# Kernel tuning notes

Measured on AMD Instinct MI355X. Metric: run time of the kernel, lower is better.

The kernel has to match this reference:

```python
import jax, jax.numpy as jnp
import numpy as np

N, D_IN, D_OUT = 4096, 1024, 1024

def setup_inputs() -> dict:
    key = jax.random.key(0)
    ks = jax.random.split(key, 7)
    s = 1.0 / np.sqrt(D_IN)
    return {
        "x": jax.random.normal(ks[0], (N, D_IN), dtype=jnp.float32),
        "W1": jax.random.normal(ks[1], (D_OUT, D_IN), dtype=jnp.float32) * s,
        "b1": jax.random.normal(ks[2], (D_OUT,), dtype=jnp.float32) * 0.01,
        "W2": jax.random.normal(ks[3], (D_OUT, D_IN), dtype=jnp.float32) * s,
        "b2": jax.random.normal(ks[4], (D_OUT,), dtype=jnp.float32) * 0.01,
        "W3": jax.random.normal(ks[5], (D_OUT, D_IN), dtype=jnp.float32) * s,
        "b3": jax.random.normal(ks[6], (D_OUT,), dtype=jnp.float32) * 0.01,
        "output_dim": D_OUT,
    }

def reference(x, W1, b1, W2, b2, W3, b3, output_dim):
    # q, k, v: [N, D_OUT]  (torch Linear: x @ W.T + b)
    q = x @ W1.T + b1
    k = x @ W2.T + b2
    v = x @ W3.T + b3
    # NOTE: original computes K @ Q^T (not Q @ K^T) — keep faithful.
    scale = 1.0 / jnp.sqrt(jnp.asarray(output_dim, dtype=x.dtype))
    attn = jax.nn.softmax(jnp.einsum("nd,md->nm", k, q) * scale, axis=-1)  # [N, N]
    # value.unsqueeze(0) * attn.unsqueeze(-1) summed over axis 1 == attn @ v
    return attn @ v  # [N, D_OUT]
```

## Files before the change

### kernel.cpp

```cpp
#include <hip/hip_runtime.h>


typedef short bf16x8 __attribute__((ext_vector_type(8)));
typedef float f32x4  __attribute__((ext_vector_type(4)));

__device__ __forceinline__ short f2bf(float f) {
    unsigned u = __builtin_bit_cast(unsigned, f);
    u += 0x7FFFu + ((u >> 16) & 1u);
    return (short)(u >> 16);
}
__device__ __forceinline__ float bf2f(short s) {
    return __builtin_bit_cast(float, (unsigned)((unsigned short)s) << 16);
}

__device__ __forceinline__ void gld_lds16(const short* g, short* l) {
    __builtin_amdgcn_global_load_lds(
        (const __attribute__((address_space(1))) void*)g,
        (__attribute__((address_space(3))) void*)l, 16, 0, 0);
}

#define WAITV(n) asm volatile("s_waitcnt vmcnt(" #n ")" ::: "memory")
#define BAR() __builtin_amdgcn_s_barrier()

template<int CMODE>
__global__ __launch_bounds__(512)
void gemm256(const short* __restrict__ A, int lda,
             const short* __restrict__ B, int ldb,
             const float* __restrict__ bias,
             short* __restrict__ Cout, int ldc, float scale,
             int K, size_t zstride)
{
    __shared__ __align__(16) short As[2][2][128 * 64];
    __shared__ __align__(16) short Bs[2][2][128 * 64];

    const int tid  = threadIdx.x;
    const int lane = tid & 63;
    const int wave = tid >> 6;
    const int wr   = wave >> 2;
    const int wc   = wave & 3;
    const int quad = lane >> 4;
    const int l16  = lane & 15;
    const size_t bm0 = (size_t)blockIdx.y * 256;
    const size_t bn0 = (size_t)blockIdx.x * 256;
    const int koff = blockIdx.z * K;

    f32x4 acc[8][4] = {};

    const int srow  = lane >> 3;
    const int sgran = (lane & 7) ^ srow;
    const short* Ag0 = A + (bm0 + wave * 16 + srow) * (size_t)lda + koff + sgran * 8;
    const short* Ag1 = Ag0 + (size_t)128 * lda;
    const short* Bg0 = B + (bn0 + wave * 16 + srow) * (size_t)ldb + koff + sgran * 8;
    const short* Bg1 = Bg0 + (size_t)128 * ldb;

    const int s0  = ((quad ^ (l16 & 7)) << 3);
    const int s1  = (((4 + quad) ^ (l16 & 7)) << 3);
    const int rdA0 = (wr * 64 + l16) * 64;
    const int rdB0 = (wc * 32 + l16) * 64;

    const int NT = K >> 6;

    auto stage = [&](short* half, const short* g, int ld, int kt) {
#pragma unroll
        for (int i = 0; i < 2; ++i)
            gld_lds16(g + (size_t)(i * 8) * ld + kt,
                      half + (wave * 16 + i * 8) * 64);
    };

    bf16x8 af[4][2], bfr0[2][2], bfr1[2][2];

    auto ldAf = [&](const short* Ah) {
#pragma unroll
        for (int m4 = 0; m4 < 4; ++m4) {
            af[m4][0] = *(const bf16x8*)(Ah + rdA0 + m4 * 1024 + s0);
            af[m4][1] = *(const bf16x8*)(Ah + rdA0 + m4 * 1024 + s1);
        }
    };
    auto ldBf = [&](bf16x8 (&bx)[2][2], const short* Bh) {
#pragma unroll
        for (int n2 = 0; n2 < 2; ++n2) {
            bx[n2][0] = *(const bf16x8*)(Bh + rdB0 + n2 * 1024 + s0);
            bx[n2][1] = *(const bf16x8*)(Bh + rdB0 + n2 * 1024 + s1);
        }
    };
    auto mm = [&](int mq, int nq, bf16x8 (&bx)[2][2]) {
        __builtin_amdgcn_s_setprio(1);
#pragma unroll
        for (int ks = 0; ks < 2; ++ks)
#pragma unroll
            for (int m4 = 0; m4 < 4; ++m4)
#pragma unroll
                for (int n2 = 0; n2 < 2; ++n2)
                    acc[mq * 4 + m4][nq * 2 + n2] =
                        __builtin_amdgcn_mfma_f32_16x16x32_bf16(
                            af[m4][ks], bx[n2][ks],
                            acc[mq * 4 + m4][nq * 2 + n2], 0, 0, 0);
        __builtin_amdgcn_s_setprio(0);
    };

    stage(&As[0][0][0], Ag0, lda, 0);
    stage(&As[0][1][0], Ag1, lda, 0);
    stage(&Bs[0][0][0], Bg0, ldb, 0);
    stage(&Bs[0][1][0], Bg1, ldb, 0);
    stage(&As[1][0][0], Ag0, lda, 64);
    stage(&Bs[1][1][0], Bg1, ldb, 64);
    WAITV(4);
    BAR();
    __builtin_amdgcn_sched_barrier(0);

    for (int it = 0; it < NT / 2; ++it) {
        const int k1 = it * 128 + 64;
        const int k2 = it * 128 + 128;
        const int k3 = it * 128 + 192;
        const bool m2 = k2 < K, m3 = k3 < K;

        ldAf(&As[0][0][0]);
        ldBf(bfr0, &Bs[0][0][0]);
        stage(&As[1][1][0], Ag1, lda, k1);
        BAR();
        mm(0, 0, bfr0);
        ldBf(bfr1, &Bs[0][1][0]);
        stage(&Bs[1][0][0], Bg0, ldb, k1);
        BAR();
        mm(0, 1, bfr1);
        ldAf(&As[0][1][0]);
        if (m2) stage(&As[0][0][0], Ag0, lda, k2);
        BAR();
        mm(1, 1, bfr1);
        if (m2) stage(&Bs[0][1][0], Bg1, ldb, k2);
        mm(1, 0, bfr0);
        if (m2) { WAITV(4); } else { WAITV(0); }
        BAR();

        ldAf(&As[1][0][0]);
        ldBf(bfr0, &Bs[1][0][0]);
        if (m2) stage(&As[0][1][0], Ag1, lda, k2);
        BAR();
        mm(0, 0, bfr0);
        ldBf(bfr1, &Bs[1][1][0]);
        if (m2) stage(&Bs[0][0][0], Bg0, ldb, k2);
        BAR();
        mm(0, 1, bfr1);
        ldAf(&As[1][1][0]);
        if (m3) stage(&As[1][0][0], Ag0, lda, k3);
        BAR();
        mm(1, 1, bfr1);
        if (m3) stage(&Bs[1][1][0], Bg1, ldb, k3);
        mm(1, 0, bfr0);
        if (m2) {
            WAITV(4);
            BAR();
        }
    }

    short* Cs = Cout + ((CMODE == 3) ? (size_t)blockIdx.z * zstride : 0);
#pragma unroll
    for (int mt = 0; mt < 8; ++mt) {
        const int mq = mt >> 2, m4 = mt & 3;
#pragma unroll
        for (int nt = 0; nt < 4; ++nt) {
            const int nq = nt >> 1, n2 = nt & 1;
            const size_t col = bn0 + nq * 128 + wc * 32 + n2 * 16 + l16;
            const float bc = (CMODE == 0) ? bias[col] : 0.0f;
#pragma unroll
            for (int r = 0; r < 4; ++r) {
                const size_t row = bm0 + mq * 128 + wr * 64 + m4 * 16 + quad * 4 + r;
                float v = acc[mt][nt][r] * scale + bc;
                if (CMODE == 2) v = __expf(v);
                Cs[row * (size_t)ldc + col] = f2bf(v);
            }
        }
    }
}

__global__ __launch_bounds__(256)
void transpose_v(const short* __restrict__ qkv, short* __restrict__ vt)
{
    __shared__ short sh[64][72];
    const int n0 = blockIdx.x * 64, d0 = blockIdx.y * 64;
    const int t = threadIdx.x;
    const int r = t >> 2, c = (t & 3) << 4;

    const short* src = qkv + (size_t)(n0 + r) * 3072 + 2048 + d0 + c;
    *(int4*)(&sh[r][c])     = *(const int4*)(src);
    *(int4*)(&sh[r][c + 8]) = *(const int4*)(src + 8);
    __syncthreads();

    short tmp[16];
#pragma unroll
    for (int j = 0; j < 16; j++) tmp[j] = sh[c + j][r];
    short* dst = vt + (size_t)(d0 + r) * 4096 + n0 + c;
    *(int4*)(dst)     = *(const int4*)(tmp);
    *(int4*)(dst + 8) = *(const int4*)(tmp + 8);
}

__global__ __launch_bounds__(256)
void reduce4div(const short* __restrict__ E, const short* __restrict__ outp,
                float* __restrict__ out)
{
    const int row = blockIdx.x;
    const int t = threadIdx.x;
    const int wave = t >> 6, lane = t & 63;

    const short* e = E + (size_t)row * 4096 + (t << 4);
    short sh[16];
    *(int4*)(sh)     = *(const int4*)(e);
    *(int4*)(sh + 8) = *(const int4*)(e + 8);
    float s = 0.0f;
#pragma unroll
    for (int i = 0; i < 16; i++) s += bf2f(sh[i]);
#pragma unroll
    for (int off = 32; off; off >>= 1) s += __shfl_down(s, off);
    __shared__ float red[4];
    if (lane == 0) red[wave] = s;
    __syncthreads();
    const float inv = 1.0f / (red[0] + red[1] + red[2] + red[3]);

    const size_t base = (size_t)row * 1024 + (t << 2);
    float a[4] = {0.0f, 0.0f, 0.0f, 0.0f};
#pragma unroll
    for (int z = 0; z < 4; z++) {
        short4 p = *(const short4*)(outp + z * (size_t)4096 * 1024 + base);
        a[0] += bf2f(p.x); a[1] += bf2f(p.y);
        a[2] += bf2f(p.z); a[3] += bf2f(p.w);
    }
    float4 o;
    o.x = a[0] * inv; o.y = a[1] * inv; o.z = a[2] * inv; o.w = a[3] * inv;
    *(float4*)(out + base) = o;
}

__global__ __launch_bounds__(256)
void prep(const float* __restrict__ x, const float* __restrict__ W1,
          const float* __restrict__ W2, const float* __restrict__ W3,
          const float* __restrict__ b1, const float* __restrict__ b2,
          const float* __restrict__ b3,
          short* __restrict__ xb, short* __restrict__ Wb,
          float* __restrict__ bcat)
{
    const int i = blockIdx.x * 256 + threadIdx.x;
    const int NX = 1048576;
    const int NW = 262144;
    if (i < NX + 3 * NW) {
        const float* src; short* dst; int j;
        if (i < NX)               { src = x;  dst = xb; j = i; }
        else if (i < NX + NW)     { src = W1; dst = Wb; j = i - NX; }
        else if (i < NX + 2 * NW) { src = W2; dst = Wb + 1048576; j = i - NX - NW; }
        else                      { src = W3; dst = Wb + 2097152; j = i - NX - 2 * NW; }
        const float4 f = ((const float4*)src)[j];
        short4 o;
        o.x = f2bf(f.x); o.y = f2bf(f.y); o.z = f2bf(f.z); o.w = f2bf(f.w);
        *(short4*)(dst + (j << 2)) = o;
    } else {
        const int j = i - (NX + 3 * NW);
        if (j < 3072)
            bcat[j] = (j < 1024) ? b1[j] : (j < 2048 ? b2[j - 1024] : b3[j - 2048]);
    }
}

extern "C" void kernel_launch(void* const* d_in, const int* in_sizes, int n_in,
                              void* d_out, int out_size, void* d_ws, size_t ws_size,
                              hipStream_t stream)
{
    const float* x  = (const float*)d_in[0];
    const float* W1 = (const float*)d_in[1];
    const float* b1 = (const float*)d_in[2];
    const float* W2 = (const float*)d_in[3];
    const float* b2 = (const float*)d_in[4];
    const float* W3 = (const float*)d_in[5];
    const float* b3 = (const float*)d_in[6];
    float* out = (float*)d_out;

    const int N = 4096, D = 1024;

    char* wsb = (char*)d_ws;
    short* vt   = (short*)wsb;
    short* E    = (short*)(wsb + (size_t)8  * 1024 * 1024);
    short* xb   = (short*)(wsb + (size_t)40 * 1024 * 1024);
    short* Wb   = (short*)(wsb + (size_t)48 * 1024 * 1024);
    float* bcat = (float*)(wsb + (size_t)54 * 1024 * 1024);
    short* qkv  = (short*)(wsb + (size_t)54 * 1024 * 1024 + 16384);
    short* outp = (short*)(wsb + (size_t)40 * 1024 * 1024);

    prep<<<(1048576 + 3 * 262144 + 3072 + 255) / 256, 256, 0, stream>>>(
        x, W1, W2, W3, b1, b2, b3, xb, Wb, bcat);

    dim3 gqkv(3 * D / 256, N / 256);
    gemm256<0><<<gqkv, 512, 0, stream>>>(xb, D, Wb, D, bcat,
                                         qkv, 3 * D, 1.0f, D, 0);

    dim3 gt(N / 64, D / 64);
    transpose_v<<<gt, 256, 0, stream>>>(qkv, vt);

    dim3 gs(N / 256, N / 256);
    gemm256<2><<<gs, 512, 0, stream>>>(qkv + D, 3 * D, qkv, 3 * D,
                                       nullptr, E, N, 0.03125f, D, 0);

    dim3 go(D / 256, N / 256, 4);
    gemm256<3><<<go, 512, 0, stream>>>(E, N, vt, N, nullptr,
                                       outp, D, 1.0f, N / 4,
                                       (size_t)N * D);

    reduce4div<<<N, 256, 0, stream>>>(E, outp, out);
}
```

Measured before the change: 219.2 us.

## Restructure GEMM main loop with peeled last iteration and explicit LDS waits

Rewrites the double-buffered GEMM K-loop so the final iteration is peeled via a compile-time flag, removing the per-iteration runtime bounds checks on staging. It reorders which LDS halves are staged when, deepens prefetch (vmcnt 6), and adds explicit lgkmcnt waits plus extra barriers around each MFMA block to control LDS read/write ordering. The extra barriers may cut overlap between waves, while the clearer schedule aims to keep global-to-LDS loads in flight longer.

```diff
diff --git a/kernel.cpp b/kernel.cpp
--- a/kernel.cpp
+++ b/kernel.cpp
@@ -3,6 +3,9 @@
 
 typedef short bf16x8 __attribute__((ext_vector_type(8)));
 typedef float f32x4  __attribute__((ext_vector_type(4)));
+
+struct FalseT { static constexpr bool value = false; };
+struct TrueT  { static constexpr bool value = true;  };
 
 __device__ __forceinline__ short f2bf(float f) {
     unsigned u = __builtin_bit_cast(unsigned, f);
@@ -20,7 +23,10 @@
 }
 
 #define WAITV(n) asm volatile("s_waitcnt vmcnt(" #n ")" ::: "memory")
-#define BAR() __builtin_amdgcn_s_barrier()
+#define LGKM0()  do { asm volatile("s_waitcnt lgkmcnt(0)" ::: "memory"); \
+                      __builtin_amdgcn_sched_barrier(0); } while (0)
+#define LGKM8()  asm volatile("s_waitcnt lgkmcnt(8)" ::: "memory")
+#define BAR()    __builtin_amdgcn_s_barrier()
 
 template<int CMODE>
 __global__ __launch_bounds__(512)
@@ -53,12 +59,10 @@
     const short* Bg0 = B + (bn0 + wave * 16 + srow) * (size_t)ldb + koff + sgran * 8;
     const short* Bg1 = Bg0 + (size_t)128 * ldb;
 
-    const int s0  = ((quad ^ (l16 & 7)) << 3);
-    const int s1  = (((4 + quad) ^ (l16 & 7)) << 3);
+    const int s0   = ((quad ^ (l16 & 7)) << 3);
+    const int s1   = (((4 + quad) ^ (l16 & 7)) << 3);
     const int rdA0 = (wr * 64 + l16) * 64;
     const int rdB0 = (wc * 32 + l16) * 64;
-
-    const int NT = K >> 6;
 
     auto stage = [&](short* half, const short* g, int ld, int kt) {
 #pragma unroll
@@ -99,59 +103,75 @@
     };
 
     stage(&As[0][0][0], Ag0, lda, 0);
-    stage(&As[0][1][0], Ag1, lda, 0);
     stage(&Bs[0][0][0], Bg0, ldb, 0);
     stage(&Bs[0][1][0], Bg1, ldb, 0);
+    stage(&As[0][1][0], Ag1, lda, 0);
     stage(&As[1][0][0], Ag0, lda, 64);
+    stage(&Bs[1][0][0], Bg0, ldb, 64);
     stage(&Bs[1][1][0], Bg1, ldb, 64);
-    WAITV(4);
+    WAITV(6);
     BAR();
     __builtin_amdgcn_sched_barrier(0);
 
-    for (int it = 0; it < NT / 2; ++it) {
-        const int k1 = it * 128 + 64;
-        const int k2 = it * 128 + 128;
-        const int k3 = it * 128 + 192;
-        const bool m2 = k2 < K, m3 = k3 < K;
-
+    int kt = 0;
+    auto iterbody = [&](auto LASTC) {
+        constexpr bool LAST = decltype(LASTC)::value;
         ldAf(&As[0][0][0]);
         ldBf(bfr0, &Bs[0][0][0]);
-        stage(&As[1][1][0], Ag1, lda, k1);
-        BAR();
+        stage(&As[1][1][0], Ag1, lda, kt + 64);
+        LGKM8();
+        BAR();
+        LGKM0();
         mm(0, 0, bfr0);
+        BAR();
         ldBf(bfr1, &Bs[0][1][0]);
-        stage(&Bs[1][0][0], Bg0, ldb, k1);
-        BAR();
+        if constexpr (!LAST) stage(&As[0][0][0], Ag0, lda, kt + 128);
+        BAR();
+        LGKM0();
         mm(0, 1, bfr1);
+        BAR();
         ldAf(&As[0][1][0]);
-        if (m2) stage(&As[0][0][0], Ag0, lda, k2);
-        BAR();
+        if constexpr (!LAST) stage(&Bs[0][0][0], Bg0, ldb, kt + 128);
+        BAR();
+        LGKM0();
         mm(1, 1, bfr1);
-        if (m2) stage(&Bs[0][1][0], Bg1, ldb, k2);
+        BAR();
+        if constexpr (!LAST) stage(&Bs[0][1][0], Bg1, ldb, kt + 128);
         mm(1, 0, bfr0);
-        if (m2) { WAITV(4); } else { WAITV(0); }
-        BAR();
-
+        if constexpr (LAST) { WAITV(0); } else { WAITV(6); }
+        BAR();
         ldAf(&As[1][0][0]);
         ldBf(bfr0, &Bs[1][0][0]);
-        if (m2) stage(&As[0][1][0], Ag1, lda, k2);
-        BAR();
+        if constexpr (!LAST) stage(&As[0][1][0], Ag1, lda, kt + 128);
+        LGKM8();
+        BAR();
+        LGKM0();
         mm(0, 0, bfr0);
+        BAR();
         ldBf(bfr1, &Bs[1][1][0]);
-        if (m2) stage(&Bs[0][0][0], Bg0, ldb, k2);
-        BAR();
+        if constexpr (!LAST) stage(&As[1][0][0], Ag0, lda, kt + 192);
+        BAR();
+        LGKM0();
         mm(0, 1, bfr1);
+        BAR();
         ldAf(&As[1][1][0]);
-        if (m3) stage(&As[1][0][0], Ag0, lda, k3);
-        BAR();
+        if constexpr (!LAST) stage(&Bs[1][0][0], Bg0, ldb, kt + 192);
+        BAR();
+        LGKM0();
         mm(1, 1, bfr1);
-        if (m3) stage(&Bs[1][1][0], Bg1, ldb, k3);
+        BAR();
+        if constexpr (!LAST) stage(&Bs[1][1][0], Bg1, ldb, kt + 192);
         mm(1, 0, bfr0);
-        if (m2) {
-            WAITV(4);
-            BAR();
-        }
+        if constexpr (!LAST) { WAITV(6); }
+        BAR();
+    };
+
+    const int nfull = (K >> 7) - 1;
+    for (int i = 0; i < nfull; ++i) {
+        iterbody(FalseT{});
+        kt += 128;
     }
+    iterbody(TrueT{});
 
     short* Cs = Cout + ((CMODE == 3) ? (size_t)blockIdx.z * zstride : 0);
 #pragma unroll
```

Result: no change. 218.0 us (-0.6%).
